# Kernel optimization log

Hardware: AMD Instinct MI355X
Metric: run time of the kernel (lower is better)

The kernel has to match this reference:

```python
import jax, jax.numpy as jnp
import numpy as np

N_NODES = 100_000
N_EDGES = 1_600_000
F_IN, H, C = 128, 128, 64


def setup_inputs() -> dict:
    key = jax.random.key(0)
    ks = jax.random.split(key, 12)
    s = 0.05  # weight init scale
    features = jax.random.normal(ks[0], (N_NODES, F_IN), jnp.float32)
    src = jax.random.randint(ks[1], (N_EDGES,), 0, N_NODES)
    dst = jax.random.randint(ks[2], (N_EDGES,), 0, N_NODES)
    return {
        "features": features,
        "src": src,
        "dst": dst,
        "Ws0": jax.random.normal(ks[3], (F_IN, H), jnp.float32) * s,
        "Wn0": jax.random.normal(ks[4], (F_IN, H), jnp.float32) * s,
        "b0": jnp.zeros((H,), jnp.float32),
        "Ws1": jax.random.normal(ks[5], (H, H), jnp.float32) * s,
        "Wn1": jax.random.normal(ks[6], (H, H), jnp.float32) * s,
        "b1": jnp.zeros((H,), jnp.float32),
        "Ws2": jax.random.normal(ks[7], (H, C), jnp.float32) * s,
        "Wn2": jax.random.normal(ks[8], (H, C), jnp.float32) * s,
        "b2": jnp.zeros((C,), jnp.float32),
    }


def sage_conv(feat, src, dst, Ws, Wn, b):
    """DGL SAGEConv with mean aggregator: fc_self(h) + fc_neigh(mean_{u->v} h_u) + b."""
    n = feat.shape[0]
    deg = jax.ops.segment_sum(jnp.ones(src.shape[0], feat.dtype), dst, num_segments=n)
    # gather src features along edges, reduce by dst (irregular gather-scatter)
    neigh = jax.ops.segment_sum(feat[src], dst, num_segments=n)
    neigh = neigh / jnp.maximum(deg, 1.0)[:, None]
    return feat @ Ws + neigh @ Wn + b


def reference(features, src, dst, Ws0, Wn0, b0, Ws1, Wn1, b1, Ws2, Wn2, b2):
    # eval mode: dropout is identity
    h = sage_conv(features, src, dst, Ws0, Wn0, b0)
    h = jax.nn.relu(h)
    h = sage_conv(h, src, dst, Ws1, Wn1, b1)
    h = jax.nn.relu(h)
    h = sage_conv(h, src, dst, Ws2, Wn2, b2)
    return h
```

## Files before the change

### kernel.cpp

```cpp
#include <hip/hip_runtime.h>

typedef _Float16 f16x8 __attribute__((ext_vector_type(8)));
typedef _Float16 f16x2 __attribute__((ext_vector_type(2)));
typedef float f32x4 __attribute__((ext_vector_type(4)));


__global__ __launch_bounds__(256) void deg_kernel(const int* __restrict__ dst,
                                                  int* __restrict__ deg, int n_edges) {
  int i = blockIdx.x * 256 + threadIdx.x;
  if (i < n_edges) atomicAdd(&deg[dst[i]], 1);
}

__global__ __launch_bounds__(256) void scan1_kernel(const int* __restrict__ deg,
                                                    int* __restrict__ incl,
                                                    int* __restrict__ bsums, int n) {
  __shared__ int buf[256];
  int tid = threadIdx.x;
  int i = blockIdx.x * 256 + tid;
  int v = (i < n) ? deg[i] : 0;
  int x = v;
  buf[tid] = x;
  __syncthreads();
#pragma unroll
  for (int off = 1; off < 256; off <<= 1) {
    int t = (tid >= off) ? buf[tid - off] : 0;
    __syncthreads();
    x += t;
    buf[tid] = x;
    __syncthreads();
  }
  if (i < n) incl[i] = x;
  if (tid == 255) bsums[blockIdx.x] = x;
}

__global__ __launch_bounds__(1024) void scan2_kernel(int* __restrict__ bsums, int nb) {
  __shared__ int buf[1024];
  int tid = threadIdx.x;
  int v = (tid < nb) ? bsums[tid] : 0;
  int x = v;
  buf[tid] = x;
  __syncthreads();
#pragma unroll
  for (int off = 1; off < 1024; off <<= 1) {
    int t = (tid >= off) ? buf[tid - off] : 0;
    __syncthreads();
    x += t;
    buf[tid] = x;
    __syncthreads();
  }
  if (tid < nb) bsums[tid] = x - v;
}

__global__ __launch_bounds__(256) void scan3_kernel(const int* __restrict__ incl,
                                                    const int* __restrict__ bexcl,
                                                    const int* __restrict__ deg,
                                                    int* __restrict__ row_ptr,
                                                    int* __restrict__ cursor, int n) {
  int i = blockIdx.x * 256 + threadIdx.x;
  if (i < n) {
    int inc = incl[i] + bexcl[i >> 8];
    row_ptr[i + 1] = inc;
    cursor[i] = inc - deg[i];
  }
  if (i == 0) row_ptr[0] = 0;
}

__global__ __launch_bounds__(256) void scatter_kernel(const int* __restrict__ src,
                                                      const int* __restrict__ dst,
                                                      int* __restrict__ cursor,
                                                      int* __restrict__ src_sorted,
                                                      int n_edges) {
  int i = blockIdx.x * 256 + threadIdx.x;
  if (i < n_edges) {
    int pos = atomicAdd(&cursor[dst[i]], 1);
    src_sorted[pos] = src[i];
  }
}

__global__ __launch_bounds__(256) void convert_features(const float* __restrict__ f,
                                                        _Float16* __restrict__ X, int n) {
  int idx = blockIdx.x * 256 + threadIdx.x;
  int total = n * 32;
  if (idx >= total) return;
  int node = idx >> 5;
  int c4 = (idx & 31) * 4;
  float4 v = *(const float4*)(f + (size_t)node * 128 + c4);
  _Float16* o = X + (size_t)node * 256 + c4;
  o[0] = (_Float16)v.x;
  o[1] = (_Float16)v.y;
  o[2] = (_Float16)v.z;
  o[3] = (_Float16)v.w;
}

__global__ __launch_bounds__(256) void build_wt(const float* __restrict__ Ws,
                                                const float* __restrict__ Wn,
                                                _Float16* __restrict__ Wt, int NOUT) {
  int idx = blockIdx.x * 256 + threadIdx.x;
  if (idx >= NOUT * 256) return;
  int nn = idx >> 8;
  int k = idx & 255;
  float v = (k < 128) ? Ws[(size_t)k * NOUT + nn] : Wn[(size_t)(k - 128) * NOUT + nn];
  Wt[(size_t)nn * 256 + k] = (_Float16)v;
}

__global__ __launch_bounds__(256) void aggregate_f16(
    const _Float16* __restrict__ X, const int* __restrict__ row_ptr,
    const int* __restrict__ src_sorted, const int* __restrict__ deg,
    _Float16* __restrict__ Xout, int n) {
  int gid = blockIdx.x * 256 + threadIdx.x;
  int node = gid >> 6;
  int lane = gid & 63;
  if (node >= n) return;
  int beg = row_ptr[node];
  int end = row_ptr[node + 1];
  float ax = 0.f, ay = 0.f;
  int e = beg;
  for (; e + 4 <= end; e += 4) {
    int s0 = src_sorted[e + 0];
    int s1 = src_sorted[e + 1];
    int s2 = src_sorted[e + 2];
    int s3 = src_sorted[e + 3];
    f16x2 v0 = *(const f16x2*)(X + (size_t)s0 * 256 + lane * 2);
    f16x2 v1 = *(const f16x2*)(X + (size_t)s1 * 256 + lane * 2);
    f16x2 v2 = *(const f16x2*)(X + (size_t)s2 * 256 + lane * 2);
    f16x2 v3 = *(const f16x2*)(X + (size_t)s3 * 256 + lane * 2);
    ax += (float)v0[0] + (float)v1[0] + (float)v2[0] + (float)v3[0];
    ay += (float)v0[1] + (float)v1[1] + (float)v2[1] + (float)v3[1];
  }
  for (; e < end; ++e) {
    int s0 = src_sorted[e];
    f16x2 v0 = *(const f16x2*)(X + (size_t)s0 * 256 + lane * 2);
    ax += (float)v0[0];
    ay += (float)v0[1];
  }
  float inv = 1.0f / fmaxf((float)deg[node], 1.0f);
  f16x2 o;
  o[0] = (_Float16)(ax * inv);
  o[1] = (_Float16)(ay * inv);
  *(f16x2*)(Xout + (size_t)node * 256 + 128 + lane * 2) = o;
}

template <int NOUT, bool RELU, bool FINAL>
__global__ __launch_bounds__(256) void gemm_mfma(
    const _Float16* __restrict__ X, const _Float16* __restrict__ Wt,
    const float* __restrict__ bias, _Float16* __restrict__ outX,
    float* __restrict__ outF, int n) {
  constexpr int CW = NOUT / 2;
  constexpr int CF = CW / 16;
  __shared__ _Float16 Xs[128][72];
  __shared__ _Float16 Wc[NOUT][72];

  int tid = threadIdx.x;
  int lane = tid & 63;
  int wid = tid >> 6;
  int wr = wid >> 1;
  int wc = wid & 1;
  int node0 = blockIdx.x * 128;

  f32x4 acc[4][CF];
#pragma unroll
  for (int i = 0; i < 4; ++i)
#pragma unroll
    for (int j = 0; j < CF; ++j) acc[i][j] = {0.f, 0.f, 0.f, 0.f};

#pragma unroll
  for (int c = 0; c < 4; ++c) {
    int k0 = c * 64;
#pragma unroll
    for (int i = 0; i < 4; ++i) {
      int idx = i * 256 + tid;
      int r = idx >> 3;
      int o = (idx & 7) * 8;
      f16x8 v;
#pragma unroll
      for (int z = 0; z < 8; ++z) v[z] = (_Float16)0.f;
      int node = node0 + r;
      if (node < n) v = *(const f16x8*)(X + (size_t)node * 256 + k0 + o);
      *(f16x8*)&Xs[r][o] = v;
    }
#pragma unroll
    for (int i = 0; i < NOUT / 32; ++i) {
      int idx = i * 256 + tid;
      int r = idx >> 3;
      int o = (idx & 7) * 8;
      *(f16x8*)&Wc[r][o] = *(const f16x8*)(Wt + (size_t)r * 256 + k0 + o);
    }
    __syncthreads();
#pragma unroll
    for (int ks = 0; ks < 2; ++ks) {
      int kk = ks * 32 + (lane >> 4) * 8;
      f16x8 a[4], b[CF];
#pragma unroll
      for (int i = 0; i < 4; ++i)
        a[i] = *(const f16x8*)&Xs[wr * 64 + i * 16 + (lane & 15)][kk];
#pragma unroll
      for (int j = 0; j < CF; ++j)
        b[j] = *(const f16x8*)&Wc[wc * CW + j * 16 + (lane & 15)][kk];
#pragma unroll
      for (int i = 0; i < 4; ++i)
#pragma unroll
        for (int j = 0; j < CF; ++j)
          acc[i][j] = __builtin_amdgcn_mfma_f32_16x16x32_f16(a[i], b[j], acc[i][j], 0, 0, 0);
    }
    __syncthreads();
  }

#pragma unroll
  for (int j = 0; j < CF; ++j) {
    int col = wc * CW + j * 16 + (lane & 15);
    float bv = bias[col];
#pragma unroll
    for (int i = 0; i < 4; ++i) {
#pragma unroll
      for (int q = 0; q < 4; ++q) {
        int row = wr * 64 + i * 16 + (lane >> 4) * 4 + q;
        int node = node0 + row;
        if (node < n) {
          float v = acc[i][j][q] + bv;
          if (RELU) v = fmaxf(v, 0.f);
          if (FINAL)
            outF[(size_t)node * NOUT + col] = v;
          else
            outX[(size_t)node * 256 + col] = (_Float16)v;
        }
      }
    }
  }
}

extern "C" void kernel_launch(void* const* d_in, const int* in_sizes, int n_in,
                              void* d_out, int out_size, void* d_ws, size_t ws_size,
                              hipStream_t stream) {
  const float* features = (const float*)d_in[0];
  const int* src = (const int*)d_in[1];
  const int* dst = (const int*)d_in[2];
  const float* Ws0 = (const float*)d_in[3];
  const float* Wn0 = (const float*)d_in[4];
  const float* b0 = (const float*)d_in[5];
  const float* Ws1 = (const float*)d_in[6];
  const float* Wn1 = (const float*)d_in[7];
  const float* b1 = (const float*)d_in[8];
  const float* Ws2 = (const float*)d_in[9];
  const float* Wn2 = (const float*)d_in[10];
  const float* b2 = (const float*)d_in[11];

  const int n = in_sizes[0] / 128;
  const int n_edges = in_sizes[1];

  char* ws = (char*)d_ws;
  size_t off = 0;
  auto alloc = [&](size_t bytes) -> void* {
    void* p = ws + off;
    off += (bytes + 255) & ~(size_t)255;
    return p;
  };
  int* deg = (int*)alloc((size_t)n * 4);
  int* row_ptr = (int*)alloc(((size_t)n + 1) * 4);
  int* cursor = (int*)alloc((size_t)n * 4);
  int* incl = (int*)alloc((size_t)n * 4);
  int* bsums = (int*)alloc(1024 * 4);
  int* src_sorted = (int*)alloc((size_t)n_edges * 4);
  _Float16* XA = (_Float16*)alloc((size_t)n * 256 * 2);
  _Float16* XB = (_Float16*)alloc((size_t)n * 256 * 2);
  _Float16* Wt0 = (_Float16*)alloc((size_t)128 * 256 * 2);
  _Float16* Wt1 = (_Float16*)alloc((size_t)128 * 256 * 2);
  _Float16* Wt2 = (_Float16*)alloc((size_t)64 * 256 * 2);

  hipMemsetAsync(deg, 0, (size_t)n * 4, stream);

  int eb = (n_edges + 255) / 256;
  int nb = (n + 255) / 256;
  deg_kernel<<<eb, 256, 0, stream>>>(dst, deg, n_edges);
  scan1_kernel<<<nb, 256, 0, stream>>>(deg, incl, bsums, n);
  scan2_kernel<<<1, 1024, 0, stream>>>(bsums, nb);
  scan3_kernel<<<nb, 256, 0, stream>>>(incl, bsums, deg, row_ptr, cursor, n);
  scatter_kernel<<<eb, 256, 0, stream>>>(src, dst, cursor, src_sorted, n_edges);

  convert_features<<<(n * 32 + 255) / 256, 256, 0, stream>>>(features, XA, n);
  build_wt<<<(128 * 256 + 255) / 256, 256, 0, stream>>>(Ws0, Wn0, Wt0, 128);
  build_wt<<<(128 * 256 + 255) / 256, 256, 0, stream>>>(Ws1, Wn1, Wt1, 128);
  build_wt<<<(64 * 256 + 255) / 256, 256, 0, stream>>>(Ws2, Wn2, Wt2, 64);

  int agg_blocks = (int)(((size_t)n * 64 + 255) / 256);
  int gemm_blocks = (n + 127) / 128;

  aggregate_f16<<<agg_blocks, 256, 0, stream>>>(XA, row_ptr, src_sorted, deg, XA, n);
  gemm_mfma<128, true, false><<<gemm_blocks, 256, 0, stream>>>(XA, Wt0, b0, XB, nullptr, n);
  aggregate_f16<<<agg_blocks, 256, 0, stream>>>(XB, row_ptr, src_sorted, deg, XB, n);
  gemm_mfma<128, true, false><<<gemm_blocks, 256, 0, stream>>>(XB, Wt1, b1, XA, nullptr, n);
  aggregate_f16<<<agg_blocks, 256, 0, stream>>>(XA, row_ptr, src_sorted, deg, XA, n);
  gemm_mfma<64, false, true><<<gemm_blocks, 256, 0, stream>>>(XA, Wt2, b2, nullptr, (float*)d_out, n);
}
```

Measured before the change: 617.9 us.

## Build CSR via two-level bucketed counting sort with LDS atomics

Replaces the global-atomic degree count, three-pass scan and global-atomic scatter with a bucketed counting sort. Edges are binned into 128-node buckets using per-block LDS histograms, scattered as packed (local dst, src) words, then sorted within each bucket in LDS to produce deg, row_ptr and src_sorted. The aim is to cut contended global atomics and random writes, at the cost of more kernel launches and an extra pass over the edge array. Packing src into 18 bits limits node count to 262144 and bucket count to 1024.

```diff
diff --git a/kernel.cpp b/kernel.cpp
--- a/kernel.cpp
+++ b/kernel.cpp
@@ -5,75 +5,132 @@
 typedef float f32x4 __attribute__((ext_vector_type(4)));
 
 
-__global__ __launch_bounds__(256) void deg_kernel(const int* __restrict__ dst,
-                                                  int* __restrict__ deg, int n_edges) {
-  int i = blockIdx.x * 256 + threadIdx.x;
-  if (i < n_edges) atomicAdd(&deg[dst[i]], 1);
-}
-
-__global__ __launch_bounds__(256) void scan1_kernel(const int* __restrict__ deg,
-                                                    int* __restrict__ incl,
-                                                    int* __restrict__ bsums, int n) {
-  __shared__ int buf[256];
-  int tid = threadIdx.x;
-  int i = blockIdx.x * 256 + tid;
-  int v = (i < n) ? deg[i] : 0;
+#define BSHIFT 7
+#define BSZ 128
+#define EPB 16384
+
+__global__ __launch_bounds__(256) void histA(const int* __restrict__ dst,
+                                             int* __restrict__ hist_pb,
+                                             int n_edges, int nbk) {
+  __shared__ unsigned lh[1024];
+  for (int i = threadIdx.x; i < nbk; i += 256) lh[i] = 0;
+  __syncthreads();
+  int base = blockIdx.x * EPB;
+  for (int i = threadIdx.x; i < EPB; i += 256) {
+    int e = base + i;
+    if (e < n_edges) atomicAdd(&lh[dst[e] >> BSHIFT], 1u);
+  }
+  __syncthreads();
+  for (int i = threadIdx.x; i < nbk; i += 256)
+    hist_pb[(size_t)blockIdx.x * nbk + i] = (int)lh[i];
+}
+
+__global__ __launch_bounds__(256) void sumB1(const int* __restrict__ hist_pb,
+                                             int* __restrict__ btot, int nblk, int nbk) {
+  int b = blockIdx.x * 256 + threadIdx.x;
+  if (b >= nbk) return;
+  int s = 0;
+  for (int k = 0; k < nblk; ++k) s += hist_pb[(size_t)k * nbk + b];
+  btot[b] = s;
+}
+
+__global__ __launch_bounds__(1024) void scanB2(const int* __restrict__ btot,
+                                               int* __restrict__ bbase, int nbk) {
+  __shared__ int buf[1024];
+  int t = threadIdx.x;
+  int v = (t < nbk) ? btot[t] : 0;
   int x = v;
-  buf[tid] = x;
-  __syncthreads();
-#pragma unroll
-  for (int off = 1; off < 256; off <<= 1) {
-    int t = (tid >= off) ? buf[tid - off] : 0;
-    __syncthreads();
-    x += t;
-    buf[tid] = x;
-    __syncthreads();
-  }
-  if (i < n) incl[i] = x;
-  if (tid == 255) bsums[blockIdx.x] = x;
-}
-
-__global__ __launch_bounds__(1024) void scan2_kernel(int* __restrict__ bsums, int nb) {
-  __shared__ int buf[1024];
-  int tid = threadIdx.x;
-  int v = (tid < nb) ? bsums[tid] : 0;
-  int x = v;
-  buf[tid] = x;
+  buf[t] = x;
   __syncthreads();
 #pragma unroll
   for (int off = 1; off < 1024; off <<= 1) {
-    int t = (tid >= off) ? buf[tid - off] : 0;
-    __syncthreads();
-    x += t;
-    buf[tid] = x;
-    __syncthreads();
-  }
-  if (tid < nb) bsums[tid] = x - v;
-}
-
-__global__ __launch_bounds__(256) void scan3_kernel(const int* __restrict__ incl,
-                                                    const int* __restrict__ bexcl,
-                                                    const int* __restrict__ deg,
-                                                    int* __restrict__ row_ptr,
-                                                    int* __restrict__ cursor, int n) {
-  int i = blockIdx.x * 256 + threadIdx.x;
-  if (i < n) {
-    int inc = incl[i] + bexcl[i >> 8];
-    row_ptr[i + 1] = inc;
-    cursor[i] = inc - deg[i];
-  }
-  if (i == 0) row_ptr[0] = 0;
-}
-
-__global__ __launch_bounds__(256) void scatter_kernel(const int* __restrict__ src,
-                                                      const int* __restrict__ dst,
-                                                      int* __restrict__ cursor,
-                                                      int* __restrict__ src_sorted,
-                                                      int n_edges) {
-  int i = blockIdx.x * 256 + threadIdx.x;
-  if (i < n_edges) {
-    int pos = atomicAdd(&cursor[dst[i]], 1);
-    src_sorted[pos] = src[i];
+    int tm = (t >= off) ? buf[t - off] : 0;
+    __syncthreads();
+    x += tm;
+    buf[t] = x;
+    __syncthreads();
+  }
+  if (t < nbk) bbase[t] = x - v;
+  if (t == nbk - 1) bbase[nbk] = x;
+}
+
+__global__ __launch_bounds__(256) void offsB3(int* __restrict__ hist_pb,
+                                              const int* __restrict__ bbase,
+                                              int nblk, int nbk) {
+  int b = blockIdx.x * 256 + threadIdx.x;
+  if (b >= nbk) return;
+  int run = bbase[b];
+  for (int k = 0; k < nblk; ++k) {
+    int t = hist_pb[(size_t)k * nbk + b];
+    hist_pb[(size_t)k * nbk + b] = run;
+    run += t;
+  }
+}
+
+__global__ __launch_bounds__(256) void scatC(const int* __restrict__ src,
+                                             const int* __restrict__ dst,
+                                             const int* __restrict__ hist_pb,
+                                             unsigned* __restrict__ pairs,
+                                             int n_edges, int nbk) {
+  __shared__ unsigned lofs[1024];
+  for (int i = threadIdx.x; i < nbk; i += 256)
+    lofs[i] = (unsigned)hist_pb[(size_t)blockIdx.x * nbk + i];
+  __syncthreads();
+  int base = blockIdx.x * EPB;
+  for (int i = threadIdx.x; i < EPB; i += 256) {
+    int e = base + i;
+    if (e < n_edges) {
+      int d = dst[e];
+      unsigned pos = atomicAdd(&lofs[d >> BSHIFT], 1u);
+      pairs[pos] = ((unsigned)(d & (BSZ - 1)) << 18) | (unsigned)src[e];
+    }
+  }
+}
+
+__global__ __launch_bounds__(256) void finalD(const unsigned* __restrict__ pairs,
+                                              const int* __restrict__ bbase,
+                                              int* __restrict__ deg,
+                                              int* __restrict__ row_ptr,
+                                              int* __restrict__ src_sorted,
+                                              int n, int nbk) {
+  __shared__ int ldeg[BSZ];
+  __shared__ int lscan[BSZ];
+  __shared__ int lcur[BSZ];
+  int b = blockIdx.x;
+  int t = threadIdx.x;
+  int node0 = b << BSHIFT;
+  int beg = bbase[b], end = bbase[b + 1];
+  if (t < BSZ) ldeg[t] = 0;
+  __syncthreads();
+  for (int i = beg + t; i < end; i += 256) atomicAdd(&ldeg[pairs[i] >> 18], 1);
+  __syncthreads();
+  int x = (t < BSZ) ? ldeg[t] : 0;
+  if (t < BSZ) lscan[t] = x;
+  __syncthreads();
+#pragma unroll
+  for (int off = 1; off < BSZ; off <<= 1) {
+    int tm = (t >= off && t < BSZ) ? lscan[t - off] : 0;
+    __syncthreads();
+    if (t < BSZ) {
+      x += tm;
+      lscan[t] = x;
+    }
+    __syncthreads();
+  }
+  if (t < BSZ) {
+    int node = node0 + t;
+    lcur[t] = beg + lscan[t] - ldeg[t];
+    if (node < n) {
+      deg[node] = ldeg[t];
+      row_ptr[node + 1] = beg + lscan[t];
+      if (node == 0) row_ptr[0] = 0;
+    }
+  }
+  __syncthreads();
+  for (int i = beg + t; i < end; i += 256) {
+    unsigned p = pairs[i];
+    int pos = atomicAdd(&lcur[p >> 18], 1);
+    src_sorted[pos] = (int)(p & 0x3FFFFu);
   }
 }
 
@@ -246,6 +303,8 @@
 
   const int n = in_sizes[0] / 128;
   const int n_edges = in_sizes[1];
+  const int nbk = (n + BSZ - 1) >> BSHIFT;
+  const int nblk = (n_edges + EPB - 1) / EPB;
 
   char* ws = (char*)d_ws;
   size_t off = 0;
@@ -254,11 +313,12 @@
     off += (bytes + 255) & ~(size_t)255;
     return p;
   };
+  int* hist_pb = (int*)alloc((size_t)nblk * nbk * 4);
+  int* btot = (int*)alloc((size_t)nbk * 4);
+  int* bbase = (int*)alloc(((size_t)nbk + 1) * 4);
+  unsigned* pairs = (unsigned*)alloc((size_t)n_edges * 4);
   int* deg = (int*)alloc((size_t)n * 4);
   int* row_ptr = (int*)alloc(((size_t)n + 1) * 4);
-  int* cursor = (int*)alloc((size_t)n * 4);
-  int* incl = (int*)alloc((size_t)n * 4);
-  int* bsums = (int*)alloc(1024 * 4);
   int* src_sorted = (int*)alloc((size_t)n_edges * 4);
   _Float16* XA = (_Float16*)alloc((size_t)n * 256 * 2);
   _Float16* XB = (_Float16*)alloc((size_t)n * 256 * 2);
@@ -266,15 +326,13 @@
   _Float16* Wt1 = (_Float16*)alloc((size_t)128 * 256 * 2);
   _Float16* Wt2 = (_Float16*)alloc((size_t)64 * 256 * 2);
 
-  hipMemsetAsync(deg, 0, (size_t)n * 4, stream);
-
-  int eb = (n_edges + 255) / 256;
-  int nb = (n + 255) / 256;
-  deg_kernel<<<eb, 256, 0, stream>>>(dst, deg, n_edges);
-  scan1_kernel<<<nb, 256, 0, stream>>>(deg, incl, bsums, n);
-  scan2_kernel<<<1, 1024, 0, stream>>>(bsums, nb);
-  scan3_kernel<<<nb, 256, 0, stream>>>(incl, bsums, deg, row_ptr, cursor, n);
-  scatter_kernel<<<eb, 256, 0, stream>>>(src, dst, cursor, src_sorted, n_edges);
+  int nbkb = (nbk + 255) / 256;
+  histA<<<nblk, 256, 0, stream>>>(dst, hist_pb, n_edges, nbk);
+  sumB1<<<nbkb, 256, 0, stream>>>(hist_pb, btot, nblk, nbk);
+  scanB2<<<1, 1024, 0, stream>>>(btot, bbase, nbk);
+  offsB3<<<nbkb, 256, 0, stream>>>(hist_pb, bbase, nblk, nbk);
+  scatC<<<nblk, 256, 0, stream>>>(src, dst, hist_pb, pairs, n_edges, nbk);
+  finalD<<<nbk, 256, 0, stream>>>(pairs, bbase, deg, row_ptr, src_sorted, n, nbk);
 
   convert_features<<<(n * 32 + 255) / 256, 256, 0, stream>>>(features, XA, n);
   build_wt<<<(128 * 256 + 255) / 256, 256, 0, stream>>>(Ws0, Wn0, Wt0, 128);
```

Result: faster. 549.3 us (-11.1%).
